# Performance work log

Measured on AMD Instinct MI355X. Metric: run time of the kernel, lower is better.

The kernel has to match this reference:

```python
import jax, jax.numpy as jnp
import numpy as np

N = 50000        # nodes
E = 800000       # edges
F_IN = 16        # num_features
F_EDGE = 8       # num_edge_features
H = 4            # heads
C = 32           # hidden_dim (per-head out channels)
D = H * C        # 128, node state width
NUM_CLASSES = 5
NEG_SLOPE = 0.2  # PyG GATConv default leaky_relu slope


def setup_inputs() -> dict:
    key = jax.random.key(0)
    ks = jax.random.split(key, 30)
    def w(k, shape):
        return jax.random.normal(k, shape, dtype=jnp.float32) * 0.05
    return {
        "x": jax.random.normal(ks[0], (N, F_IN), dtype=jnp.float32),
        "edge_index": jax.random.randint(ks[1], (2, E), 0, N),
        "edge_attr": jax.random.normal(ks[2], (E, F_EDGE), dtype=jnp.float32),
        # edge_encoder: Linear(F_EDGE->C), ReLU, Linear(C->H)
        "ee_w1": w(ks[3], (C, F_EDGE)), "ee_b1": jnp.zeros((C,), jnp.float32),
        "ee_w2": w(ks[4], (H, C)),      "ee_b2": jnp.zeros((H,), jnp.float32),
        # input_proj: Linear(F_IN -> D)
        "proj_w": w(ks[5], (D, F_IN)), "proj_b": jnp.zeros((D,), jnp.float32),
        # conv1: GATConv(F_IN, C, heads=H, edge_dim=H, concat=True)
        "c1_lin": w(ks[6], (D, F_IN)),
        "c1_att_src": w(ks[7], (H, C)), "c1_att_dst": w(ks[8], (H, C)),
        "c1_lin_edge": w(ks[9], (D, H)), "c1_att_edge": w(ks[10], (H, C)),
        "c1_bias": jnp.zeros((D,), jnp.float32),
        # conv2: GATConv(D, C, heads=H, edge_dim=H, concat=True)
        "c2_lin": w(ks[11], (D, D)),
        "c2_att_src": w(ks[12], (H, C)), "c2_att_dst": w(ks[13], (H, C)),
        "c2_lin_edge": w(ks[14], (D, H)), "c2_att_edge": w(ks[15], (H, C)),
        "c2_bias": jnp.zeros((D,), jnp.float32),
        # layer norms
        "n1_g": jnp.ones((D,), jnp.float32), "n1_b": jnp.zeros((D,), jnp.float32),
        "n2_g": jnp.ones((D,), jnp.float32), "n2_b": jnp.zeros((D,), jnp.float32),
        # jk_proj: Linear(3D -> D)
        "jk_w": w(ks[16], (D, 3 * D)), "jk_b": jnp.zeros((D,), jnp.float32),
        # classifier: Linear(D -> NUM_CLASSES)
        "cls_w": w(ks[17], (NUM_CLASSES, D)), "cls_b": jnp.zeros((NUM_CLASSES,), jnp.float32),
    }


def _layer_norm(h, g, b, eps=1e-5):
    mu = jnp.mean(h, axis=-1, keepdims=True)
    var = jnp.var(h, axis=-1, keepdims=True)
    return (h - mu) * jax.lax.rsqrt(var + eps) * g + b


def _gat_conv(x, src, dst, e_attr, lin_w, att_src, att_dst, lin_edge_w, att_edge, bias):
    """PyG GATConv (v1) with edge features, concat=True, eval mode (no dropout)."""
    n = x.shape[0]
    xs = (x @ lin_w.T).reshape(n, H, C)                      # [N,H,C]
    a_src = jnp.einsum('nhc,hc->nh', xs, att_src)            # [N,H]
    a_dst = jnp.einsum('nhc,hc->nh', xs, att_dst)            # [N,H]
    ee = (e_attr @ lin_edge_w.T).reshape(-1, H, C)           # [E,H,C]
    a_edge = jnp.einsum('ehc,hc->eh', ee, att_edge)          # [E,H]
    alpha = jax.nn.leaky_relu(a_src[src] + a_dst[dst] + a_edge, NEG_SLOPE)
    # segment softmax over destination neighborhoods
    amax = jax.ops.segment_max(alpha, dst, num_segments=n)
    ex = jnp.exp(alpha - amax[dst])
    denom = jax.ops.segment_sum(ex, dst, num_segments=n)
    alpha = ex / (denom[dst] + 1e-16)                        # [E,H]
    msg = xs[src] * alpha[:, :, None]                        # [E,H,C]
    out = jax.ops.segment_sum(msg, dst, num_segments=n)      # [N,H,C]
    return out.reshape(n, H * C) + bias


def reference(x, edge_index, edge_attr,
              ee_w1, ee_b1, ee_w2, ee_b2,
              proj_w, proj_b,
              c1_lin, c1_att_src, c1_att_dst, c1_lin_edge, c1_att_edge, c1_bias,
              c2_lin, c2_att_src, c2_att_dst, c2_lin_edge, c2_att_edge, c2_bias,
              n1_g, n1_b, n2_g, n2_b,
              jk_w, jk_b, cls_w, cls_b):
    src, dst = edge_index[0], edge_index[1]
    # edge encoder
    e = jax.nn.relu(edge_attr @ ee_w1.T + ee_b1) @ ee_w2.T + ee_b2   # [E,H]
    h0 = x @ proj_w.T + proj_b                                        # [N,D]
    h1 = _gat_conv(x, src, dst, e, c1_lin, c1_att_src, c1_att_dst,
                   c1_lin_edge, c1_att_edge, c1_bias)
    h1 = _layer_norm(jax.nn.elu(h1) + h0, n1_g, n1_b)
    h2 = _gat_conv(h1, src, dst, e, c2_lin, c2_att_src, c2_att_dst,
                   c2_lin_edge, c2_att_edge, c2_bias)
    h2 = _layer_norm(jax.nn.elu(h2) + h1, n2_g, n2_b)
    h = jnp.concatenate([h0, h1, h2], axis=-1) @ jk_w.T + jk_b
    out = h @ cls_w.T + cls_b
    return jax.nn.log_softmax(out, axis=1)
```

## Files before the change

### kernel.cpp

```cpp
#include <hip/hip_runtime.h>
#include <cstdint>

#define NN 50000
#define NE 800000

using short8  = __attribute__((ext_vector_type(8))) short;
using float4v = __attribute__((ext_vector_type(4))) float;

__device__ __forceinline__ ushort f2bf(float f) {
    uint u = __float_as_uint(f);
    uint r = (u + 0x7fffu + ((u >> 16) & 1u)) >> 16;
    return (ushort)r;
}
__device__ __forceinline__ float bf2f(uint u) {
    return __uint_as_float(u << 16);
}

__global__ __launch_bounds__(256) void k_prep2(const float* __restrict__ le1, const float* __restrict__ ae1,
                                               const float* __restrict__ le2, const float* __restrict__ ae2,
                                               const float* __restrict__ jkw, const float* __restrict__ jkb,
                                               const float* __restrict__ clw, const float* __restrict__ clb,
                                               const float* __restrict__ projw, const float* __restrict__ c1lin,
                                               const float* __restrict__ c2lin,
                                               const float* __restrict__ asrc1, const float* __restrict__ adst1,
                                               float* __restrict__ M, float* __restrict__ CW,
                                               float* __restrict__ cbp,
                                               ushort* __restrict__ w01b, ushort* __restrict__ c2b,
                                               float* __restrict__ Vmat, int* __restrict__ deg)
{
    int idx = blockIdx.x * 256 + threadIdx.x;
    if (idx < NN) deg[idx] = 0;
    if (idx < 32) {
        const float* le = (idx < 16) ? le1 : le2;
        const float* ae = (idx < 16) ? ae1 : ae2;
        int hk = idx & 15, h = hk >> 2, k = hk & 3;
        float s = 0.f;
        for (int c = 0; c < 32; ++c)
            s += le[(h * 32 + c) * 4 + k] * ae[h * 32 + c];
        M[idx] = s;
    } else if (idx < 1952) {
        int o = idx - 32;
        int r = o / 384, c = o - r * 384;
        float s = 0.f;
        for (int k = 0; k < 128; ++k)
            s += clw[r * 128 + k] * jkw[(size_t)k * 384 + c];
        CW[o] = s;
    } else if (idx < 1957) {
        int r = idx - 1952;
        float s = clb[r];
        for (int k = 0; k < 128; ++k)
            s += clw[r * 128 + k] * jkb[k];
        cbp[r] = s;
    } else if (idx >= 2048 && idx < 10240) {
        int o = idx - 2048;
        int r = o >> 5, c = o & 31;
        float v = 0.f;
        if (c < 16) v = (r < 128) ? projw[r * 16 + c] : c1lin[(r - 128) * 16 + c];
        w01b[o] = f2bf(v);
    } else if (idx >= 10240 && idx < 26624) {
        int o = idx - 10240;
        c2b[o] = f2bf(c2lin[o]);
    } else if (idx >= 26624 && idx < 26752) {
        int o = idx - 26624;
        const float* att = (o < 64) ? asrc1 : adst1;
        int oo = o & 63, h = oo >> 4, k = oo & 15;
        float s = 0.f;
        for (int c = 0; c < 32; ++c)
            s += c1lin[(h * 32 + c) * 16 + k] * att[h * 32 + c];
        Vmat[o] = s;
    }
}

__global__ __launch_bounds__(256) void k_att1(const float* __restrict__ x,
                                              const float* __restrict__ V,
                                              float* __restrict__ as_o,
                                              float* __restrict__ ad_o)
{
    __shared__ float sV[128];
    int t = threadIdx.x;
    if (t < 128) sV[t] = V[t];
    __syncthreads();
    int n = blockIdx.x * 256 + t;
    if (n >= NN) return;
    const float4* xr = (const float4*)(x + (size_t)n * 16);
    float4 x0 = xr[0], x1 = xr[1], x2 = xr[2], x3 = xr[3];
    float xv[16] = {x0.x,x0.y,x0.z,x0.w, x1.x,x1.y,x1.z,x1.w,
                    x2.x,x2.y,x2.z,x2.w, x3.x,x3.y,x3.z,x3.w};
    float s[4], d[4];
    #pragma unroll
    for (int h = 0; h < 4; ++h) {
        float ss = 0.f, dd = 0.f;
        #pragma unroll
        for (int k = 0; k < 16; ++k) {
            ss += xv[k] * sV[h * 16 + k];
            dd += xv[k] * sV[64 + h * 16 + k];
        }
        s[h] = ss; d[h] = dd;
    }
    *(float4*)(as_o + (size_t)n * 4) = make_float4(s[0], s[1], s[2], s[3]);
    *(float4*)(ad_o + (size_t)n * 4) = make_float4(d[0], d[1], d[2], d[3]);
}

__global__ __launch_bounds__(256) void k_edge_mlp(const float* __restrict__ ea,
                                                  const float* __restrict__ w1,
                                                  const float* __restrict__ b1,
                                                  const float* __restrict__ w2,
                                                  const float* __restrict__ b2,
                                                  const int* __restrict__ ei,
                                                  const float* __restrict__ Mm,
                                                  const float* __restrict__ as1,
                                                  const float* __restrict__ ad1,
                                                  int* __restrict__ deg,
                                                  ushort* __restrict__ exb,
                                                  float4* __restrict__ ae2)
{
    __shared__ float sw1[256], sb1[32], sw2[128], sb2[4], sM[32];
    int t = threadIdx.x;
    sw1[t] = w1[t];
    if (t < 128) sw2[t] = w2[t];
    if (t < 32)  { sb1[t] = b1[t]; sM[t] = Mm[t]; }
    if (t < 4)   sb2[t] = b2[t];
    __syncthreads();
    int e = blockIdx.x * 256 + t;
    if (e >= NE) return;
    int src = ei[e], dst = ei[NE + e];
    float4 s4 = *(const float4*)(as1 + (size_t)src * 4);
    float4 d4 = *(const float4*)(ad1 + (size_t)dst * 4);
    float4 x0 = *(const float4*)(ea + (size_t)e * 8);
    float4 x1 = *(const float4*)(ea + (size_t)e * 8 + 4);
    float o0 = sb2[0], o1 = sb2[1], o2 = sb2[2], o3 = sb2[3];
    #pragma unroll
    for (int j = 0; j < 32; ++j) {
        const float* w = sw1 + j * 8;
        float s = sb1[j] + w[0]*x0.x + w[1]*x0.y + w[2]*x0.z + w[3]*x0.w
                         + w[4]*x1.x + w[5]*x1.y + w[6]*x1.z + w[7]*x1.w;
        s = fmaxf(s, 0.f);
        o0 += sw2[0*32+j] * s; o1 += sw2[1*32+j] * s;
        o2 += sw2[2*32+j] * s; o3 += sw2[3*32+j] * s;
    }
    atomicAdd(&deg[dst], 1);
    float sa[4] = {s4.x, s4.y, s4.z, s4.w};
    float da[4] = {d4.x, d4.y, d4.z, d4.w};
    ushort exq[4];
    float a2[4];
    #pragma unroll
    for (int h = 0; h < 4; ++h) {
        float ae1 = sM[h*4+0]*o0 + sM[h*4+1]*o1 + sM[h*4+2]*o2 + sM[h*4+3]*o3;
        float al = sa[h] + da[h] + ae1;
        al = al > 0.f ? al : 0.2f * al;
        exq[h] = f2bf(__expf(al));
        a2[h] = sM[16+h*4+0]*o0 + sM[16+h*4+1]*o1 + sM[16+h*4+2]*o2 + sM[16+h*4+3]*o3;
    }
    *(uint2*)(exb + (size_t)e * 4) =
        make_uint2((uint)exq[0] | ((uint)exq[1] << 16), (uint)exq[2] | ((uint)exq[3] << 16));
    ae2[e] = make_float4(a2[0], a2[1], a2[2], a2[3]);
}

__global__ __launch_bounds__(256) void k_scan_blk(const int* __restrict__ deg,
                                                  int* __restrict__ loc,
                                                  int* __restrict__ bsum)
{
    __shared__ int tmp[256];
    int t = threadIdx.x;
    int i = blockIdx.x * 256 + t;
    int v = (i < NN) ? deg[i] : 0;
    tmp[t] = v;
    __syncthreads();
    #pragma unroll
    for (int o = 1; o < 256; o <<= 1) {
        int add = (t >= o) ? tmp[t - o] : 0;
        __syncthreads();
        tmp[t] += add;
        __syncthreads();
    }
    if (i < NN) loc[i] = tmp[t] - v;
    if (t == 255) bsum[blockIdx.x] = tmp[255];
}

__global__ __launch_bounds__(256) void k_scan_top(const int* __restrict__ bsum,
                                                  int* __restrict__ bcarry,
                                                  int* __restrict__ total_out, int nb)
{
    __shared__ int tmp[256];
    int t = threadIdx.x;
    int v = (t < nb) ? bsum[t] : 0;
    tmp[t] = v;
    __syncthreads();
    #pragma unroll
    for (int o = 1; o < 256; o <<= 1) {
        int add = (t >= o) ? tmp[t - o] : 0;
        __syncthreads();
        tmp[t] += add;
        __syncthreads();
    }
    if (t < nb) bcarry[t] = tmp[t] - v;
    if (t == 255) *total_out = tmp[255];
}

__global__ __launch_bounds__(256) void k_scan_add(const int* __restrict__ loc,
                                                  const int* __restrict__ bcarry,
                                                  int* __restrict__ off,
                                                  int* __restrict__ cur)
{
    int i = blockIdx.x * 256 + threadIdx.x;
    if (i < NN) {
        int o = loc[i] + bcarry[blockIdx.x];
        off[i] = o;
        cur[i] = o;
    }
}

__global__ __launch_bounds__(256) void k_scatter2(const int* __restrict__ ei,
                                                  int* __restrict__ cursor,
                                                  int2* __restrict__ csr2)
{
    int e = blockIdx.x * 256 + threadIdx.x;
    if (e >= NE) return;
    int src = ei[e], dst = ei[NE + e];
    int p = atomicAdd(&cursor[dst], 1);
    csr2[p] = make_int2(src, e);
}

__global__ __launch_bounds__(256) void k_gemm1(const float* __restrict__ x,
                                               const ushort* __restrict__ w01,
                                               const float* __restrict__ pbias,
                                               ushort* __restrict__ hcatb,
                                               ushort* __restrict__ xs, int M)
{
    int t = threadIdx.x;
    int wv = t >> 6, lane = t & 63;
    int quad = lane >> 4, r16 = lane & 15;
    int m0 = blockIdx.x * 128 + wv * 32;
    int ar0 = m0 + r16;      if (ar0 >= M) ar0 = M - 1;
    int ar1 = m0 + 16 + r16; if (ar1 >= M) ar1 = M - 1;
    short8 a0 = (short8){0,0,0,0,0,0,0,0}, a1 = a0;
    if (quad < 2) {
        const float* p0 = x + (size_t)ar0 * 16 + quad * 8;
        const float* p1 = x + (size_t)ar1 * 16 + quad * 8;
        float4 u0 = *(const float4*)p0, u1 = *(const float4*)(p0 + 4);
        float4 v0 = *(const float4*)p1, v1 = *(const float4*)(p1 + 4);
        a0[0]=(short)f2bf(u0.x); a0[1]=(short)f2bf(u0.y); a0[2]=(short)f2bf(u0.z); a0[3]=(short)f2bf(u0.w);
        a0[4]=(short)f2bf(u1.x); a0[5]=(short)f2bf(u1.y); a0[6]=(short)f2bf(u1.z); a0[7]=(short)f2bf(u1.w);
        a1[0]=(short)f2bf(v0.x); a1[1]=(short)f2bf(v0.y); a1[2]=(short)f2bf(v0.z); a1[3]=(short)f2bf(v0.w);
        a1[4]=(short)f2bf(v1.x); a1[5]=(short)f2bf(v1.y); a1[6]=(short)f2bf(v1.z); a1[7]=(short)f2bf(v1.w);
    }
    float4v acc[2][16];
    #pragma unroll
    for (int i = 0; i < 2; ++i)
        #pragma unroll
        for (int j = 0; j < 16; ++j) acc[i][j] = (float4v){0.f, 0.f, 0.f, 0.f};
    #pragma unroll
    for (int nt = 0; nt < 16; ++nt) {
        short8 b = *(const short8*)(w01 + (size_t)(nt * 16 + r16) * 32 + quad * 8);
        acc[0][nt] = __builtin_amdgcn_mfma_f32_16x16x32_bf16(a0, b, acc[0][nt], 0, 0, 0);
        acc[1][nt] = __builtin_amdgcn_mfma_f32_16x16x32_bf16(a1, b, acc[1][nt], 0, 0, 0);
    }
    #pragma unroll
    for (int rt = 0; rt < 2; ++rt) {
        #pragma unroll
        for (int nt = 0; nt < 16; ++nt) {
            int col = (nt & 7) * 16 + r16;
            float bv = (nt < 8) ? pbias[col] : 0.f;
            #pragma unroll
            for (int r = 0; r < 4; ++r) {
                int row = m0 + rt * 16 + quad * 4 + r;
                if (row < M) {
                    float v = acc[rt][nt][r] + bv;
                    if (nt < 8) hcatb[(size_t)row * 384 + col] = f2bf(v);
                    else        xs[(size_t)row * 128 + col] = f2bf(v);
                }
            }
        }
    }
}

__global__ __launch_bounds__(256) void gemm_bf16(const ushort* __restrict__ A, int lda, int K,
                                                 const ushort* __restrict__ W, int ldw,
                                                 ushort* __restrict__ Cb, int ldcb, int M)
{
    int t = threadIdx.x;
    int wv = t >> 6, lane = t & 63;
    int quad = lane >> 4, r16 = lane & 15;
    int m0 = blockIdx.x * 128 + wv * 32;
    float4v acc[2][8];
    #pragma unroll
    for (int i = 0; i < 2; ++i)
        #pragma unroll
        for (int j = 0; j < 8; ++j) acc[i][j] = (float4v){0.f, 0.f, 0.f, 0.f};
    int ar0 = m0 + r16;      if (ar0 >= M) ar0 = M - 1;
    int ar1 = m0 + 16 + r16; if (ar1 >= M) ar1 = M - 1;
    const ushort* a0p = A + (size_t)ar0 * lda + quad * 8;
    const ushort* a1p = A + (size_t)ar1 * lda + quad * 8;
    const ushort* wp  = W + (size_t)r16 * ldw + quad * 8;
    for (int k0 = 0; k0 < K; k0 += 32) {
        short8 a0 = *(const short8*)(a0p + k0);
        short8 a1 = *(const short8*)(a1p + k0);
        #pragma unroll
        for (int nt = 0; nt < 8; ++nt) {
            short8 b = *(const short8*)(wp + (size_t)(nt * 16) * ldw + k0);
            acc[0][nt] = __builtin_amdgcn_mfma_f32_16x16x32_bf16(a0, b, acc[0][nt], 0, 0, 0);
            acc[1][nt] = __builtin_amdgcn_mfma_f32_16x16x32_bf16(a1, b, acc[1][nt], 0, 0, 0);
        }
    }
    #pragma unroll
    for (int rt = 0; rt < 2; ++rt) {
        #pragma unroll
        for (int nt = 0; nt < 8; ++nt) {
            int col = nt * 16 + r16;
            #pragma unroll
            for (int r = 0; r < 4; ++r) {
                int row = m0 + rt * 16 + quad * 4 + r;
                if (row < M)
                    Cb[(size_t)row * ldcb + col] = f2bf(acc[rt][nt][r]);
            }
        }
    }
}

__global__ __launch_bounds__(256) void k_att_reduce(const ushort* __restrict__ xs,
                                                    const float* __restrict__ att_src,
                                                    const float* __restrict__ att_dst,
                                                    float* __restrict__ as_out,
                                                    float* __restrict__ ad_out)
{
    __shared__ float ssrc[128], sdst[128];
    int t = threadIdx.x;
    if (t < 128) { ssrc[t] = att_src[t]; sdst[t] = att_dst[t]; }
    __syncthreads();
    int n = blockIdx.x * 256 + t;
    if (n >= NN) return;
    float s[4] = {0,0,0,0}, d[4] = {0,0,0,0};
    const uint2* xr = (const uint2*)(xs + (size_t)n * 128);
    #pragma unroll
    for (int q = 0; q < 32; ++q) {
        uint2 p = xr[q];
        float v0 = bf2f(p.x & 0xffffu), v1 = bf2f(p.x >> 16);
        float v2 = bf2f(p.y & 0xffffu), v3 = bf2f(p.y >> 16);
        int h = q >> 3;
        const float* aw = ssrc + q * 4;
        const float* dw = sdst + q * 4;
        s[h] += v0*aw[0] + v1*aw[1] + v2*aw[2] + v3*aw[3];
        d[h] += v0*dw[0] + v1*dw[1] + v2*dw[2] + v3*dw[3];
    }
    *(float4*)(as_out + (size_t)n * 4) = make_float4(s[0], s[1], s[2], s[3]);
    *(float4*)(ad_out + (size_t)n * 4) = make_float4(d[0], d[1], d[2], d[3]);
}

__global__ __launch_bounds__(256) void k_edge_soft2(const int* __restrict__ ei,
                                                    const float* __restrict__ as_in,
                                                    const float* __restrict__ ad_in,
                                                    const float4* __restrict__ ae2,
                                                    ushort* __restrict__ exb)
{
    int e = blockIdx.x * 256 + threadIdx.x;
    if (e >= NE) return;
    int src = ei[e], dst = ei[NE + e];
    float4 s4 = *(const float4*)(as_in + (size_t)src * 4);
    float4 d4 = *(const float4*)(ad_in + (size_t)dst * 4);
    float4 a = ae2[e];
    float sa[4] = {s4.x, s4.y, s4.z, s4.w};
    float da[4] = {d4.x, d4.y, d4.z, d4.w};
    float av[4] = {a.x, a.y, a.z, a.w};
    ushort exq[4];
    #pragma unroll
    for (int h = 0; h < 4; ++h) {
        float al = sa[h] + da[h] + av[h];
        al = al > 0.f ? al : 0.2f * al;
        exq[h] = f2bf(__expf(al));
    }
    *(uint2*)(exb + (size_t)e * 4) =
        make_uint2((uint)exq[0] | ((uint)exq[1] << 16), (uint)exq[2] | ((uint)exq[3] << 16));
}

__global__ __launch_bounds__(256) void k_agg2(const int* __restrict__ off,
                                              const int2* __restrict__ csr2,
                                              const ushort* __restrict__ exb,
                                              const ushort* __restrict__ xs,
                                              const float* __restrict__ bias,
                                              const ushort* __restrict__ residb,
                                              const float* __restrict__ g,
                                              const float* __restrict__ bln,
                                              ushort* __restrict__ outb)
{
    int wave = threadIdx.x >> 6;
    int lane = threadIdx.x & 63;
    int n = blockIdx.x * 4 + wave;
    if (n >= NN) return;
    int i0 = off[n], i1 = off[n + 1];
    int c0 = lane * 2;
    int h = lane >> 4;
    float a0 = 0.f, a1 = 0.f, den = 0.f;
    int i = i0;
    for (; i + 4 <= i1; i += 4) {
        int2 se0 = csr2[i], se1 = csr2[i+1], se2 = csr2[i+2], se3 = csr2[i+3];
        float w0 = bf2f(exb[(size_t)se0.y * 4 + h]);
        float w1 = bf2f(exb[(size_t)se1.y * 4 + h]);
        float w2 = bf2f(exb[(size_t)se2.y * 4 + h]);
        float w3 = bf2f(exb[(size_t)se3.y * 4 + h]);
        uint p0 = *(const uint*)(xs + (size_t)se0.x * 128 + c0);
        uint p1 = *(const uint*)(xs + (size_t)se1.x * 128 + c0);
        uint p2 = *(const uint*)(xs + (size_t)se2.x * 128 + c0);
        uint p3 = *(const uint*)(xs + (size_t)se3.x * 128 + c0);
        a0 = fmaf(bf2f(p0 & 0xffffu), w0, a0); a1 = fmaf(bf2f(p0 >> 16), w0, a1);
        a0 = fmaf(bf2f(p1 & 0xffffu), w1, a0); a1 = fmaf(bf2f(p1 >> 16), w1, a1);
        a0 = fmaf(bf2f(p2 & 0xffffu), w2, a0); a1 = fmaf(bf2f(p2 >> 16), w2, a1);
        a0 = fmaf(bf2f(p3 & 0xffffu), w3, a0); a1 = fmaf(bf2f(p3 >> 16), w3, a1);
        den += (w0 + w1) + (w2 + w3);
    }
    for (; i < i1; ++i) {
        int2 se0 = csr2[i];
        float w0 = bf2f(exb[(size_t)se0.y * 4 + h]);
        uint p0 = *(const uint*)(xs + (size_t)se0.x * 128 + c0);
        a0 = fmaf(bf2f(p0 & 0xffffu), w0, a0);
        a1 = fmaf(bf2f(p0 >> 16), w0, a1);
        den += w0;
    }
    float inv = 1.f / (den + 1e-16f);
    float v0 = a0 * inv + bias[c0];
    float v1 = a1 * inv + bias[c0 + 1];
    v0 = v0 > 0.f ? v0 : (__expf(v0) - 1.f);
    v1 = v1 > 0.f ? v1 : (__expf(v1) - 1.f);
    uint rp = *(const uint*)(residb + (size_t)n * 384 + c0);
    float r0 = v0 + bf2f(rp & 0xffffu);
    float r1 = v1 + bf2f(rp >> 16);
    float ssum = r0 + r1, ssq = r0 * r0 + r1 * r1;
    #pragma unroll
    for (int o = 1; o < 64; o <<= 1) {
        ssum += __shfl_xor(ssum, o, 64);
        ssq  += __shfl_xor(ssq, o, 64);
    }
    float mu = ssum * (1.f / 128.f);
    float var = ssq * (1.f / 128.f) - mu * mu;
    float rs = rsqrtf(var + 1e-5f);
    float o0 = (r0 - mu) * rs * g[c0] + bln[c0];
    float o1 = (r1 - mu) * rs * g[c0 + 1] + bln[c0 + 1];
    uint pk = (uint)f2bf(o0) | ((uint)f2bf(o1) << 16);
    *(uint*)(outb + (size_t)n * 384 + c0) = pk;
}

__global__ __launch_bounds__(256) void k_cls(const ushort* __restrict__ hcatb,
                                             const float* __restrict__ CW,
                                             const float* __restrict__ cbp,
                                             float* __restrict__ out)
{
    __shared__ float sCW[1920], scb[5];
    int t = threadIdx.x;
    for (int i = t; i < 1920; i += 256) sCW[i] = CW[i];
    if (t < 5) scb[t] = cbp[t];
    __syncthreads();
    int n = blockIdx.x * 256 + t;
    if (n >= NN) return;
    float acc[5] = {scb[0], scb[1], scb[2], scb[3], scb[4]};
    const uint2* hr = (const uint2*)(hcatb + (size_t)n * 384);
    #pragma unroll 4
    for (int q = 0; q < 96; ++q) {
        uint2 p = hr[q];
        float v0 = bf2f(p.x & 0xffffu), v1 = bf2f(p.x >> 16);
        float v2 = bf2f(p.y & 0xffffu), v3 = bf2f(p.y >> 16);
        #pragma unroll
        for (int o = 0; o < 5; ++o) {
            const float* w = sCW + o * 384 + q * 4;
            acc[o] += v0*w[0] + v1*w[1] + v2*w[2] + v3*w[3];
        }
    }
    float m = acc[0];
    #pragma unroll
    for (int o = 1; o < 5; ++o) m = fmaxf(m, acc[o]);
    float sum = 0.f;
    #pragma unroll
    for (int o = 0; o < 5; ++o) sum += __expf(acc[o] - m);
    float lse = __logf(sum) + m;
    float* op = out + (size_t)n * 5;
    #pragma unroll
    for (int o = 0; o < 5; ++o) op[o] = acc[o] - lse;
}

extern "C" void kernel_launch(void* const* d_in, const int* in_sizes, int n_in,
                              void* d_out, int out_size, void* d_ws, size_t ws_size,
                              hipStream_t stream)
{
    (void)in_sizes; (void)n_in; (void)out_size; (void)ws_size;
    const float* x        = (const float*)d_in[0];
    const int*   ei       = (const int*)d_in[1];
    const float* eattr    = (const float*)d_in[2];
    const float* ee_w1    = (const float*)d_in[3];
    const float* ee_b1    = (const float*)d_in[4];
    const float* ee_w2    = (const float*)d_in[5];
    const float* ee_b2    = (const float*)d_in[6];
    const float* proj_w   = (const float*)d_in[7];
    const float* proj_b   = (const float*)d_in[8];
    const float* c1_lin   = (const float*)d_in[9];
    const float* c1_asrc  = (const float*)d_in[10];
    const float* c1_adst  = (const float*)d_in[11];
    const float* c1_ledge = (const float*)d_in[12];
    const float* c1_aedge = (const float*)d_in[13];
    const float* c1_bias  = (const float*)d_in[14];
    const float* c2_lin   = (const float*)d_in[15];
    const float* c2_asrc  = (const float*)d_in[16];
    const float* c2_adst  = (const float*)d_in[17];
    const float* c2_ledge = (const float*)d_in[18];
    const float* c2_aedge = (const float*)d_in[19];
    const float* c2_bias  = (const float*)d_in[20];
    const float* n1_g     = (const float*)d_in[21];
    const float* n1_b     = (const float*)d_in[22];
    const float* n2_g     = (const float*)d_in[23];
    const float* n2_b     = (const float*)d_in[24];
    const float* jk_w     = (const float*)d_in[25];
    const float* jk_b     = (const float*)d_in[26];
    const float* cls_w    = (const float*)d_in[27];
    const float* cls_b    = (const float*)d_in[28];
    float* out = (float*)d_out;
    float* ws  = (float*)d_ws;

    const size_t oM   = 0;
    const size_t oCW  = 64;
    const size_t oCB  = 1984;
    const size_t oV   = 2048;
    const size_t oEX  = 2176;
    const size_t oAE2 = oEX + (size_t)NE * 2;
    const size_t oHB  = oAE2 + (size_t)NE * 4;
    const size_t oXS  = oHB + (size_t)NN * 192;
    const size_t oWB  = oXS + (size_t)NN * 64;
    const size_t oAS  = oWB + 12288;
    const size_t oAD  = oAS + (size_t)NN * 4;
    const size_t oI   = oAD + (size_t)NN * 4;

    float*  Mmat  = ws + oM;
    float*  CW    = ws + oCW;
    float*  cbp   = ws + oCB;
    float*  Vmat  = ws + oV;
    ushort* exb   = (ushort*)(ws + oEX);
    float4* ae2   = (float4*)(ws + oAE2);
    ushort* hcatb = (ushort*)(ws + oHB);
    ushort* xs    = (ushort*)(ws + oXS);
    ushort* w01b  = (ushort*)(ws + oWB);
    ushort* c2b   = w01b + 8192;
    float*  as_b  = ws + oAS;
    float*  ad_b  = ws + oAD;
    int*    ip    = (int*)(ws + oI);
    int*    deg   = ip;
    int*    loc   = ip + NN;
    int*    off   = ip + 2 * NN;
    int*    cur   = ip + 3 * NN + 16;
    int*    bsum  = ip + 4 * NN + 16;
    int*    bcar  = ip + 4 * NN + 272;
    int2*   csr2  = (int2*)(ip + 4 * NN + 528);

    const int EB  = (NE + 255) / 256;
    const int NB  = (NN + 255) / 256;
    const int GB  = (NN + 127) / 128;
    const int WB2 = (NN + 3) / 4;

    k_prep2<<<NB, 256, 0, stream>>>(c1_ledge, c1_aedge, c2_ledge, c2_aedge,
                                    jk_w, jk_b, cls_w, cls_b,
                                    proj_w, c1_lin, c2_lin, c1_asrc, c1_adst,
                                    Mmat, CW, cbp, w01b, c2b, Vmat, deg);
    k_att1<<<NB, 256, 0, stream>>>(x, Vmat, as_b, ad_b);
    k_edge_mlp<<<EB, 256, 0, stream>>>(eattr, ee_w1, ee_b1, ee_w2, ee_b2, ei,
                                       Mmat, as_b, ad_b, deg, exb, ae2);
    k_scan_blk<<<NB, 256, 0, stream>>>(deg, loc, bsum);
    k_scan_top<<<1, 256, 0, stream>>>(bsum, bcar, off + NN, NB);
    k_scan_add<<<NB, 256, 0, stream>>>(loc, bcar, off, cur);
    k_scatter2<<<EB, 256, 0, stream>>>(ei, cur, csr2);

    k_gemm1<<<GB, 256, 0, stream>>>(x, w01b, proj_b, hcatb, xs, NN);

    k_agg2<<<WB2, 256, 0, stream>>>(off, csr2, exb, xs, c1_bias, hcatb,
                                    n1_g, n1_b, hcatb + 128);

    gemm_bf16<<<GB, 256, 0, stream>>>(hcatb + 128, 384, 128, c2b, 128, xs, 128, NN);
    k_att_reduce<<<NB, 256, 0, stream>>>(xs, c2_asrc, c2_adst, as_b, ad_b);
    k_edge_soft2<<<EB, 256, 0, stream>>>(ei, as_b, ad_b, ae2, exb);
    k_agg2<<<WB2, 256, 0, stream>>>(off, csr2, exb, xs, c2_bias, hcatb + 128,
                                    n2_g, n2_b, hcatb + 256);

    k_cls<<<NB, 256, 0, stream>>>(hcatb, CW, cbp, out);
}
```

Before: 398.0 us.

## Partition CSR build by destination range, fuse attention reduce into GEMM, store ae2 as bf16

The degree histogram and CSR scatter move into dedicated kernels. Each block loops over 2048 edges, and only atomics for destinations in one of 8 node ranges are issued per block, to improve atomic locality in L2. The per-node attention dot products for layer 2 are fused into the GEMM epilogue with wave shuffles, which removes the separate reduce kernel and its re-read of xs. The second-layer edge attention term is stored as bf16 instead of fp32, halving that traffic. The cost is that each edge index is read 8 times in the partitioned kernels, and the edge term loses some precision.

Measured after the change: 394.5 us. About the same (-0.9%).

```diff
diff --git a/kernel.cpp b/kernel.cpp
--- a/kernel.cpp
+++ b/kernel.cpp
@@ -3,6 +3,8 @@
 
 #define NN 50000
 #define NE 800000
+#define DPX 6250
+#define SLICES 391
 
 using short8  = __attribute__((ext_vector_type(8))) short;
 using float4v = __attribute__((ext_vector_type(4))) float;
@@ -110,9 +112,8 @@
                                                   const float* __restrict__ Mm,
                                                   const float* __restrict__ as1,
                                                   const float* __restrict__ ad1,
-                                                  int* __restrict__ deg,
                                                   ushort* __restrict__ exb,
-                                                  float4* __restrict__ ae2)
+                                                  ushort* __restrict__ ae2)
 {
     __shared__ float sw1[256], sb1[32], sw2[128], sb2[4], sM[32];
     int t = threadIdx.x;
@@ -138,22 +139,35 @@
         o0 += sw2[0*32+j] * s; o1 += sw2[1*32+j] * s;
         o2 += sw2[2*32+j] * s; o3 += sw2[3*32+j] * s;
     }
-    atomicAdd(&deg[dst], 1);
     float sa[4] = {s4.x, s4.y, s4.z, s4.w};
     float da[4] = {d4.x, d4.y, d4.z, d4.w};
-    ushort exq[4];
-    float a2[4];
+    ushort exq[4], a2q[4];
     #pragma unroll
     for (int h = 0; h < 4; ++h) {
         float ae1 = sM[h*4+0]*o0 + sM[h*4+1]*o1 + sM[h*4+2]*o2 + sM[h*4+3]*o3;
         float al = sa[h] + da[h] + ae1;
         al = al > 0.f ? al : 0.2f * al;
         exq[h] = f2bf(__expf(al));
-        a2[h] = sM[16+h*4+0]*o0 + sM[16+h*4+1]*o1 + sM[16+h*4+2]*o2 + sM[16+h*4+3]*o3;
+        a2q[h] = f2bf(sM[16+h*4+0]*o0 + sM[16+h*4+1]*o1 + sM[16+h*4+2]*o2 + sM[16+h*4+3]*o3);
     }
     *(uint2*)(exb + (size_t)e * 4) =
         make_uint2((uint)exq[0] | ((uint)exq[1] << 16), (uint)exq[2] | ((uint)exq[3] << 16));
-    ae2[e] = make_float4(a2[0], a2[1], a2[2], a2[3]);
+    *(uint2*)(ae2 + (size_t)e * 4) =
+        make_uint2((uint)a2q[0] | ((uint)a2q[1] << 16), (uint)a2q[2] | ((uint)a2q[3] << 16));
+}
+
+__global__ __launch_bounds__(256) void k_hist8(const int* __restrict__ ei, int* __restrict__ deg)
+{
+    int grp = blockIdx.x & 7;
+    int base = (blockIdx.x >> 3) * 2048 + threadIdx.x;
+    #pragma unroll
+    for (int k = 0; k < 8; ++k) {
+        int e = base + k * 256;
+        if (e < NE) {
+            int dst = ei[NE + e];
+            if (dst / DPX == grp) atomicAdd(&deg[dst], 1);
+        }
+    }
 }
 
 __global__ __launch_bounds__(256) void k_scan_blk(const int* __restrict__ deg,
@@ -210,15 +224,24 @@
     }
 }
 
-__global__ __launch_bounds__(256) void k_scatter2(const int* __restrict__ ei,
+__global__ __launch_bounds__(256) void k_scatter8(const int* __restrict__ ei,
                                                   int* __restrict__ cursor,
                                                   int2* __restrict__ csr2)
 {
-    int e = blockIdx.x * 256 + threadIdx.x;
-    if (e >= NE) return;
-    int src = ei[e], dst = ei[NE + e];
-    int p = atomicAdd(&cursor[dst], 1);
-    csr2[p] = make_int2(src, e);
+    int grp = blockIdx.x & 7;
+    int base = (blockIdx.x >> 3) * 2048 + threadIdx.x;
+    #pragma unroll
+    for (int k = 0; k < 8; ++k) {
+        int e = base + k * 256;
+        if (e < NE) {
+            int dst = ei[NE + e];
+            if (dst / DPX == grp) {
+                int src = ei[e];
+                int p = atomicAdd(&cursor[dst], 1);
+                csr2[p] = make_int2(src, e);
+            }
+        }
+    }
 }
 
 __global__ __launch_bounds__(256) void k_gemm1(const float* __restrict__ x,
@@ -274,11 +297,18 @@
     }
 }
 
-__global__ __launch_bounds__(256) void gemm_bf16(const ushort* __restrict__ A, int lda, int K,
-                                                 const ushort* __restrict__ W, int ldw,
-                                                 ushort* __restrict__ Cb, int ldcb, int M)
-{
+__global__ __launch_bounds__(256) void k_gemm2(const ushort* __restrict__ A,
+                                               const ushort* __restrict__ W,
+                                               const float* __restrict__ atts,
+                                               const float* __restrict__ attd,
+                                               ushort* __restrict__ xs,
+                                               float* __restrict__ as_o,
+                                               float* __restrict__ ad_o, int M)
+{
+    __shared__ float sAs[128], sAd[128];
     int t = threadIdx.x;
+    if (t < 128) { sAs[t] = atts[t]; sAd[t] = attd[t]; }
+    __syncthreads();
     int wv = t >> 6, lane = t & 63;
     int quad = lane >> 4, r16 = lane & 15;
     int m0 = blockIdx.x * 128 + wv * 32;
@@ -289,15 +319,16 @@
         for (int j = 0; j < 8; ++j) acc[i][j] = (float4v){0.f, 0.f, 0.f, 0.f};
     int ar0 = m0 + r16;      if (ar0 >= M) ar0 = M - 1;
     int ar1 = m0 + 16 + r16; if (ar1 >= M) ar1 = M - 1;
-    const ushort* a0p = A + (size_t)ar0 * lda + quad * 8;
-    const ushort* a1p = A + (size_t)ar1 * lda + quad * 8;
-    const ushort* wp  = W + (size_t)r16 * ldw + quad * 8;
-    for (int k0 = 0; k0 < K; k0 += 32) {
+    const ushort* a0p = A + (size_t)ar0 * 384 + quad * 8;
+    const ushort* a1p = A + (size_t)ar1 * 384 + quad * 8;
+    const ushort* wp  = W + (size_t)r16 * 128 + quad * 8;
+    #pragma unroll
+    for (int k0 = 0; k0 < 128; k0 += 32) {
         short8 a0 = *(const short8*)(a0p + k0);
         short8 a1 = *(const short8*)(a1p + k0);
         #pragma unroll
         for (int nt = 0; nt < 8; ++nt) {
-            short8 b = *(const short8*)(wp + (size_t)(nt * 16) * ldw + k0);
+            short8 b = *(const short8*)(wp + (size_t)(nt * 16) * 128 + k0);
             acc[0][nt] = __builtin_amdgcn_mfma_f32_16x16x32_bf16(a0, b, acc[0][nt], 0, 0, 0);
             acc[1][nt] = __builtin_amdgcn_mfma_f32_16x16x32_bf16(a1, b, acc[1][nt], 0, 0, 0);
         }
@@ -311,45 +342,39 @@
             for (int r = 0; r < 4; ++r) {
                 int row = m0 + rt * 16 + quad * 4 + r;
                 if (row < M)
-                    Cb[(size_t)row * ldcb + col] = f2bf(acc[rt][nt][r]);
+                    xs[(size_t)row * 128 + col] = f2bf(acc[rt][nt][r]);
             }
         }
-    }
-}
-
-__global__ __launch_bounds__(256) void k_att_reduce(const ushort* __restrict__ xs,
-                                                    const float* __restrict__ att_src,
-                                                    const float* __restrict__ att_dst,
-                                                    float* __restrict__ as_out,
-                                                    float* __restrict__ ad_out)
-{
-    __shared__ float ssrc[128], sdst[128];
-    int t = threadIdx.x;
-    if (t < 128) { ssrc[t] = att_src[t]; sdst[t] = att_dst[t]; }
-    __syncthreads();
-    int n = blockIdx.x * 256 + t;
-    if (n >= NN) return;
-    float s[4] = {0,0,0,0}, d[4] = {0,0,0,0};
-    const uint2* xr = (const uint2*)(xs + (size_t)n * 128);
-    #pragma unroll
-    for (int q = 0; q < 32; ++q) {
-        uint2 p = xr[q];
-        float v0 = bf2f(p.x & 0xffffu), v1 = bf2f(p.x >> 16);
-        float v2 = bf2f(p.y & 0xffffu), v3 = bf2f(p.y >> 16);
-        int h = q >> 3;
-        const float* aw = ssrc + q * 4;
-        const float* dw = sdst + q * 4;
-        s[h] += v0*aw[0] + v1*aw[1] + v2*aw[2] + v3*aw[3];
-        d[h] += v0*dw[0] + v1*dw[1] + v2*dw[2] + v3*dw[3];
-    }
-    *(float4*)(as_out + (size_t)n * 4) = make_float4(s[0], s[1], s[2], s[3]);
-    *(float4*)(ad_out + (size_t)n * 4) = make_float4(d[0], d[1], d[2], d[3]);
+        #pragma unroll
+        for (int r = 0; r < 4; ++r) {
+            int row = m0 + rt * 16 + quad * 4 + r;
+            float sh[4], dh[4];
+            #pragma unroll
+            for (int h = 0; h < 4; ++h) {
+                int cA = h * 32 + r16, cB = cA + 16;
+                sh[h] = acc[rt][2*h][r] * sAs[cA] + acc[rt][2*h+1][r] * sAs[cB];
+                dh[h] = acc[rt][2*h][r] * sAd[cA] + acc[rt][2*h+1][r] * sAd[cB];
+            }
+            #pragma unroll
+            for (int o = 1; o < 16; o <<= 1) {
+                #pragma unroll
+                for (int h = 0; h < 4; ++h) {
+                    sh[h] += __shfl_xor(sh[h], o, 64);
+                    dh[h] += __shfl_xor(dh[h], o, 64);
+                }
+            }
+            if (r16 == 0 && row < M) {
+                *(float4*)(as_o + (size_t)row * 4) = make_float4(sh[0], sh[1], sh[2], sh[3]);
+                *(float4*)(ad_o + (size_t)row * 4) = make_float4(dh[0], dh[1], dh[2], dh[3]);
+            }
+        }
+    }
 }
 
 __global__ __launch_bounds__(256) void k_edge_soft2(const int* __restrict__ ei,
                                                     const float* __restrict__ as_in,
                                                     const float* __restrict__ ad_in,
-                                                    const float4* __restrict__ ae2,
+                                                    const ushort* __restrict__ ae2,
                                                     ushort* __restrict__ exb)
 {
     int e = blockIdx.x * 256 + threadIdx.x;
@@ -357,10 +382,10 @@
     int src = ei[e], dst = ei[NE + e];
     float4 s4 = *(const float4*)(as_in + (size_t)src * 4);
     float4 d4 = *(const float4*)(ad_in + (size_t)dst * 4);
-    float4 a = ae2[e];
+    uint2 aq = *(const uint2*)(ae2 + (size_t)e * 4);
+    float av[4] = {bf2f(aq.x & 0xffffu), bf2f(aq.x >> 16), bf2f(aq.y & 0xffffu), bf2f(aq.y >> 16)};
     float sa[4] = {s4.x, s4.y, s4.z, s4.w};
     float da[4] = {d4.x, d4.y, d4.z, d4.w};
-    float av[4] = {a.x, a.y, a.z, a.w};
     ushort exq[4];
     #pragma unroll
     for (int h = 0; h < 4; ++h) {
@@ -518,7 +543,7 @@
     const size_t oV   = 2048;
     const size_t oEX  = 2176;
     const size_t oAE2 = oEX + (size_t)NE * 2;
-    const size_t oHB  = oAE2 + (size_t)NE * 4;
+    const size_t oHB  = oAE2 + (size_t)NE * 2;
     const size_t oXS  = oHB + (size_t)NN * 192;
     const size_t oWB  = oXS + (size_t)NN * 64;
     const size_t oAS  = oWB + 12288;
@@ -530,7 +555,7 @@
     float*  cbp   = ws + oCB;
     float*  Vmat  = ws + oV;
     ushort* exb   = (ushort*)(ws + oEX);
-    float4* ae2   = (float4*)(ws + oAE2);
+    ushort* ae2b  = (ushort*)(ws + oAE2);
     ushort* hcatb = (ushort*)(ws + oHB);
     ushort* xs    = (ushort*)(ws + oXS);
     ushort* w01b  = (ushort*)(ws + oWB);
@@ -550,27 +575,30 @@
     const int NB  = (NN + 255) / 256;
     const int GB  = (NN + 127) / 128;
     const int WB2 = (NN + 3) / 4;
+    const int PB  = SLICES * 8;
 
     k_prep2<<<NB, 256, 0, stream>>>(c1_ledge, c1_aedge, c2_ledge, c2_aedge,
                                     jk_w, jk_b, cls_w, cls_b,
                                     proj_w, c1_lin, c2_lin, c1_asrc, c1_adst,
                                     Mmat, CW, cbp, w01b, c2b, Vmat, deg);
-    k_att1<<<NB, 256, 0, stream>>>(x, Vmat, as_b, ad_b);
-    k_edge_mlp<<<EB, 256, 0, stream>>>(eattr, ee_w1, ee_b1, ee_w2, ee_b2, ei,
-                                       Mmat, as_b, ad_b, deg, exb, ae2);
+    k_hist8<<<PB, 256, 0, stream>>>(ei, deg);
     k_scan_blk<<<NB, 256, 0, stream>>>(deg, loc, bsum);
     k_scan_top<<<1, 256, 0, stream>>>(bsum, bcar, off + NN, NB);
     k_scan_add<<<NB, 256, 0, stream>>>(loc, bcar, off, cur);
-    k_scatter2<<<EB, 256, 0, stream>>>(ei, cur, csr2);
+    k_scatter8<<<PB, 256, 0, stream>>>(ei, cur, csr2);
+
+    k_att1<<<NB, 256, 0, stream>>>(x, Vmat, as_b, ad_b);
+    k_edge_mlp<<<EB, 256, 0, stream>>>(eattr, ee_w1, ee_b1, ee_w2, ee_b2, ei,
+                                       Mmat, as_b, ad_b, exb, ae2b);
 
     k_gemm1<<<GB, 256, 0, stream>>>(x, w01b, proj_b, hcatb, xs, NN);
 
     k_agg2<<<WB2, 256, 0, stream>>>(off, csr2, exb, xs, c1_bias, hcatb,
                                     n1_g, n1_b, hcatb + 128);
 
-    gemm_bf16<<<GB, 256, 0, stream>>>(hcatb + 128, 384, 128, c2b, 128, xs, 128, NN);
-    k_att_reduce<<<NB, 256, 0, stream>>>(xs, c2_asrc, c2_adst, as_b, ad_b);
-    k_edge_soft2<<<EB, 256, 0, stream>>>(ei, as_b, ad_b, ae2, exb);
+    k_gemm2<<<GB, 256, 0, stream>>>(hcatb + 128, c2b, c2_asrc, c2_adst,
+                                    xs, as_b, ad_b, NN);
+    k_edge_soft2<<<EB, 256, 0, stream>>>(ei, as_b, ad_b, ae2b, exb);
     k_agg2<<<WB2, 256, 0, stream>>>(off, csr2, exb, xs, c2_bias, hcatb + 128,
                                     n2_g, n2_b, hcatb + 256);
 
```
